# Performance work log

Measured on AMD Instinct MI355X. Metric: run time of the kernel, lower is better.

## Reference

```python
import jax, jax.numpy as jnp
import numpy as np

N_NODES = 100000
N_TYPES = 7
N_EDGES = 400000
D = 128


def setup_inputs() -> dict:
    key = jax.random.key(0)
    k1, k2, k3, k4 = jax.random.split(key, 4)
    x = jax.random.normal(k1, (N_NODES, D), dtype=jnp.float32)
    edge_indices = jax.random.randint(k2, (N_TYPES, 2, N_EDGES), 0, N_NODES, dtype=jnp.int64)
    # per-type linear weights of the cloned base GNNs (scaled for stability)
    W = jax.random.normal(k3, (N_TYPES, D, D), dtype=jnp.float32) * (1.0 / np.sqrt(D))
    b = jax.random.normal(k4, (N_TYPES, D), dtype=jnp.float32) * 0.02
    return {"x": x, "edge_indices": edge_indices, "W": W, "b": b}


def _type_conv(x, src, dst, Wt, bt, n_nodes):
    # gather -> segment-mean aggregate -> linear, one edge type
    msg = x[src]                                                   # [E, D]
    summed = jax.ops.segment_sum(msg, dst, num_segments=n_nodes)   # [N, D]
    cnt = jax.ops.segment_sum(jnp.ones(src.shape, x.dtype), dst, num_segments=n_nodes)
    mean = summed / jnp.maximum(cnt, 1.0)[:, None]
    return mean @ Wt + bt


def reference(x, edge_indices, W, b):
    n_nodes = x.shape[0]
    n_types = edge_indices.shape[0]
    # loop over the small fixed set of edge types (structurally distinct GNNs)
    acc = jnp.zeros_like(x)
    for t in range(n_types):
        acc = acc + _type_conv(x, edge_indices[t, 0], edge_indices[t, 1], W[t], b[t], n_nodes)
    return acc / n_types
```

## Files before the change

### kernel.cpp

```cpp
#include <hip/hip_runtime.h>

#define N_NODES 100000
#define N_TYPES 7
#define N_EDGES 400000
#define DIM 128
#define NTOT (N_TYPES * N_NODES)
#define ETOT (N_TYPES * N_EDGES)

#define RBITS 10
#define RNODE 1024
#define NBUCK 98
#define BSTRIDE 128
#define CAP 6144
#define CHUNK 2048
#define NCHUNKS ((N_EDGES + CHUNK - 1) / CHUNK)

typedef short v8s __attribute__((ext_vector_type(8)));
typedef float v4f __attribute__((ext_vector_type(4)));

__device__ __forceinline__ unsigned short f2bf(float f) {
    unsigned int x = __float_as_uint(f);
    return (unsigned short)((x + 0x7FFFu + ((x >> 16) & 1u)) >> 16);
}

__global__ __launch_bounds__(256) void cast_x_kernel(
    const float* __restrict__ x, unsigned short* __restrict__ xb)
{
    int i = blockIdx.x * 256 + threadIdx.x;
    if (i >= N_NODES * DIM / 4) return;
    float4 v = reinterpret_cast<const float4*>(x)[i];
    ushort4 o;
    o.x = f2bf(v.x); o.y = f2bf(v.y); o.z = f2bf(v.z); o.w = f2bf(v.w);
    reinterpret_cast<ushort4*>(xb)[i] = o;
}

__global__ __launch_bounds__(256) void cast_wt_bsum_kernel(
    const float* __restrict__ W, const float* __restrict__ b,
    unsigned short* __restrict__ WT, float* __restrict__ bsum)
{
    if (blockIdx.x == 448) {
        int j = threadIdx.x;
        if (j < DIM) {
            float s = 0.f;
            for (int t = 0; t < N_TYPES; ++t) s += b[t * DIM + j];
            bsum[j] = s;
        }
        return;
    }
    int i = blockIdx.x * 256 + threadIdx.x;
    if (i >= N_TYPES * DIM * DIM) return;
    int t = i >> 14, r = i & 16383, j = r >> 7, k = r & 127;
    WT[i] = f2bf(W[(t << 14) + (k << 7) + j]);
}

__global__ __launch_bounds__(256) void binpass_kernel(
    const int* __restrict__ ei, int* __restrict__ gcur,
    unsigned int* __restrict__ bucketbuf)
{
    __shared__ unsigned int packedLds[CHUNK];
    __shared__ unsigned char bLds[CHUNK];
    __shared__ unsigned int sortedLds[CHUNK];
    __shared__ int cnt[BSTRIDE];
    __shared__ int lofs[BSTRIDE];
    __shared__ int gbase[BSTRIDE];

    const int blk = blockIdx.x;
    const int t = blk / NCHUNKS;
    const int c = blk - t * NCHUNKS;
    const int* srcp = ei + (size_t)t * 2 * N_EDGES;
    const int* dstp = srcp + N_EDGES;
    const int e0 = c * CHUNK;
    const int e1 = min(e0 + CHUNK, N_EDGES);
    const int tid = threadIdx.x;

    if (tid < BSTRIDE) cnt[tid] = 0;
    __syncthreads();

#pragma unroll
    for (int k = 0; k < CHUNK / 256; ++k) {
        int j = tid + k * 256;
        int e = e0 + j;
        unsigned char b = 0xFF;
        unsigned int pk = 0;
        if (e < e1) {
            int s = srcp[e];
            int d = dstp[e];
            b = (unsigned char)(d >> RBITS);
            pk = ((unsigned int)(d & (RNODE - 1)) << 17) | (unsigned int)s;
            atomicAdd(&cnt[b], 1);
        }
        packedLds[j] = pk;
        bLds[j] = b;
    }
    __syncthreads();

    if (tid < BSTRIDE) lofs[tid] = cnt[tid];
    __syncthreads();
    for (int off = 1; off < BSTRIDE; off <<= 1) {
        int tv = 0;
        if (tid >= off && tid < BSTRIDE) tv = lofs[tid - off];
        __syncthreads();
        if (tid < BSTRIDE) lofs[tid] += tv;
        __syncthreads();
    }
    if (tid < BSTRIDE) lofs[tid] -= cnt[tid];
    __syncthreads();

    if (tid < BSTRIDE) {
        int n = cnt[tid];
        int base = -1;
        if (n > 0 && tid < NBUCK) {
            int rel = atomicAdd(&gcur[t * BSTRIDE + tid], n);
            base = (t * BSTRIDE + tid) * CAP + rel;
        }
        gbase[tid] = base;
        cnt[tid] = lofs[tid];
    }
    __syncthreads();

#pragma unroll
    for (int k = 0; k < CHUNK / 256; ++k) {
        int j = tid + k * 256;
        unsigned char b = bLds[j];
        if (b != 0xFF) {
            int p = atomicAdd(&cnt[b], 1);
            sortedLds[p] = packedLds[j];
        }
    }
    __syncthreads();

    const int wave = tid >> 6, lane = tid & 63;
    for (int b = wave * 32; b < wave * 32 + 32; ++b) {
        if (b >= NBUCK) break;
        int base = gbase[b];
        if (base < 0) continue;
        int o = lofs[b];
        int n = cnt[b] - o;
        for (int i = lane; i < n; i += 64)
            bucketbuf[(size_t)base + i] = sortedLds[o + i];
    }
}

__global__ __launch_bounds__(256) void bucket_hist_scan_kernel(
    const unsigned int* __restrict__ bucketbuf, const int* __restrict__ gcur,
    int* __restrict__ offs, int* __restrict__ bscan)
{
    __shared__ int cnt[RNODE];
    __shared__ int s[256];
    const int blk = blockIdx.x;
    const int t = blk / NBUCK;
    const int b = blk - t * NBUCK;
    const int n = min(gcur[t * BSTRIDE + b], CAP);
    const int g0 = b << RBITS;
    const int validR = min(RNODE, N_NODES - g0);
    const int tid = threadIdx.x;
    for (int j = tid; j < RNODE; j += 256) cnt[j] = 0;
    __syncthreads();
    const unsigned int* bb = bucketbuf + (size_t)(t * BSTRIDE + b) * CAP;
    for (int i = tid; i < n; i += 256)
        atomicAdd(&cnt[bb[i] >> 17], 1);
    __syncthreads();
    int base4 = tid * 4;
    int v[4], tot = 0;
#pragma unroll
    for (int k = 0; k < 4; ++k) { v[k] = cnt[base4 + k]; tot += v[k]; }
    s[tid] = tot;
    __syncthreads();
    for (int off = 1; off < 256; off <<= 1) {
        int t2 = (tid >= off) ? s[tid - off] : 0;
        __syncthreads();
        s[tid] += t2;
        __syncthreads();
    }
    int run = s[tid] - tot;
    int* og = offs + (size_t)t * N_NODES + g0;
#pragma unroll
    for (int k = 0; k < 4; ++k) {
        if (base4 + k < validR) og[base4 + k] = run;
        run += v[k];
    }
    if (tid == 255) bscan[t * NBUCK + b] = s[255];
}

__global__ __launch_bounds__(1024) void scan2_kernel(int* __restrict__ bsum, int nb)
{
    __shared__ int s[1024];
    int tid = threadIdx.x;
    int v = (tid < nb) ? bsum[tid] : 0;
    s[tid] = v;
    __syncthreads();
    for (int off = 1; off < 1024; off <<= 1) {
        int t2 = (tid >= off) ? s[tid - off] : 0;
        __syncthreads();
        s[tid] += t2;
        __syncthreads();
    }
    if (tid < nb) bsum[tid] = s[tid] - v;
}

__global__ __launch_bounds__(256) void scan3_kernel(
    int* __restrict__ offs, const int* __restrict__ bscan)
{
    int i = blockIdx.x * 256 + threadIdx.x;
    if (i < NTOT) {
        int t = i / N_NODES;
        int r = i - t * N_NODES;
        offs[i] += bscan[t * NBUCK + (r >> RBITS)];
    }
    if (i == 0) offs[NTOT] = ETOT;
}

__global__ __launch_bounds__(256) void place_kernel(
    const unsigned int* __restrict__ bucketbuf, const int* __restrict__ gcur,
    const int* __restrict__ offs, int* __restrict__ srcperm)
{
    __shared__ int cur[RNODE];
    __shared__ int sorted[CAP];
    const int blk = blockIdx.x;
    const int t = blk / NBUCK;
    const int b = blk - t * NBUCK;
    const int n = min(gcur[t * BSTRIDE + b], CAP);
    const int g0 = b << RBITS;
    const int validR = min(RNODE, N_NODES - g0);
    const int tid = threadIdx.x;
    const int* offt = offs + (size_t)t * N_NODES + g0;
    const int base0 = offt[0];
    for (int j = tid; j < validR; j += 256) cur[j] = offt[j] - base0;
    __syncthreads();
    const unsigned int* bb = bucketbuf + (size_t)(t * BSTRIDE + b) * CAP;
    for (int i = tid; i < n; i += 256) {
        unsigned int pk = bb[i];
        int p = atomicAdd(&cur[pk >> 17], 1);
        sorted[p] = (int)(pk & 0x1FFFFu);
    }
    __syncthreads();
    int* outp = srcperm + base0;
    for (int i = tid; i < n; i += 256) outp[i] = sorted[i];
}

__global__ __launch_bounds__(256) void aggregate_kernel(
    const unsigned short* __restrict__ xb,
    const int* __restrict__ offs,
    const int* __restrict__ srcperm,
    unsigned short* __restrict__ meanout,
    int grp0, int ngrp)
{
    int gi = blockIdx.x * 16 + (threadIdx.x >> 4);
    if (gi >= ngrp) return;
    int grp = grp0 + gi;
    int l = threadIdx.x & 15;

    int beg = offs[grp];
    int end = offs[grp + 1];
    int m = end - beg;

    int mm = m;
    mm = max(mm, __shfl_xor(mm, 16));
    mm = max(mm, __shfl_xor(mm, 32));

    float a[8];
#pragma unroll
    for (int j = 0; j < 8; ++j) a[j] = 0.f;

    const int eSafe = min(beg, ETOT - 1);
#pragma unroll 4
    for (int i = 0; i < mm; ++i) {
        bool valid = i < m;
        int e = valid ? (beg + i) : eSafe;
        int s = srcperm[e];
        uint4 v = *reinterpret_cast<const uint4*>(
            reinterpret_cast<const char*>(xb) + ((size_t)s << 8) + (l << 4));
        float w = valid ? 1.f : 0.f;
        a[0] += w * __uint_as_float(v.x << 16);
        a[1] += w * __uint_as_float(v.x & 0xFFFF0000u);
        a[2] += w * __uint_as_float(v.y << 16);
        a[3] += w * __uint_as_float(v.y & 0xFFFF0000u);
        a[4] += w * __uint_as_float(v.z << 16);
        a[5] += w * __uint_as_float(v.z & 0xFFFF0000u);
        a[6] += w * __uint_as_float(v.w << 16);
        a[7] += w * __uint_as_float(v.w & 0xFFFF0000u);
    }

    float inv = 1.0f / fmaxf((float)m, 1.0f);
    unsigned int p0, p1, p2, p3;
    asm("v_cvt_pk_bf16_f32 %0, %1, %2" : "=v"(p0) : "v"(a[0] * inv), "v"(a[1] * inv));
    asm("v_cvt_pk_bf16_f32 %0, %1, %2" : "=v"(p1) : "v"(a[2] * inv), "v"(a[3] * inv));
    asm("v_cvt_pk_bf16_f32 %0, %1, %2" : "=v"(p2) : "v"(a[4] * inv), "v"(a[5] * inv));
    asm("v_cvt_pk_bf16_f32 %0, %1, %2" : "=v"(p3) : "v"(a[6] * inv), "v"(a[7] * inv));
    uint4 o = make_uint4(p0, p1, p2, p3);
    *reinterpret_cast<uint4*>(
        reinterpret_cast<char*>(meanout) + ((size_t)gi << 8) + (l << 4)) = o;
}

__global__ __launch_bounds__(256) void matmul_kernel(
    const unsigned short* __restrict__ meanall, size_t meanStride,
    int t0, int nt,
    const unsigned short* __restrict__ WT,
    const float* __restrict__ bsum,
    float* __restrict__ out, int accum)
{
    __shared__ unsigned short sB[DIM * DIM];

    const int tid = threadIdx.x;
    const int wave = tid >> 6;
    const int lane = tid & 63;
    const int rlo = lane & 15;
    const int khi = lane >> 4;
    const int row0 = blockIdx.x * 64 + wave * 16;

    v4f acc[8];
#pragma unroll
    for (int n = 0; n < 8; ++n) acc[n] = (v4f){0.f, 0.f, 0.f, 0.f};

    for (int tt = 0; tt < nt; ++tt) {
        int t = t0 + tt;
        __syncthreads();
        const uint4* gw = reinterpret_cast<const uint4*>(WT + ((size_t)t << 14));
#pragma unroll
        for (int i = 0; i < 8; ++i) {
            int c = tid + (i << 8);
            uint4 v = gw[c];
            int L = c << 4;
            int row = L >> 8;
            int sb = (row << 8) | ((L & 255) ^ ((row & 7) << 4));
            *reinterpret_cast<uint4*>(reinterpret_cast<char*>(sB) + sb) = v;
        }
        __syncthreads();

        int rowA = row0 + rlo;
        if (rowA >= N_NODES) rowA = N_NODES - 1;
        const unsigned short* arow = meanall + (size_t)tt * meanStride + ((size_t)rowA << 7);

#pragma unroll
        for (int k0 = 0; k0 < DIM; k0 += 32) {
            v8s a = *reinterpret_cast<const v8s*>(arow + k0 + (khi << 3));
#pragma unroll
            for (int n = 0; n < 8; ++n) {
                int jrow = (n << 4) | rlo;
                int kb = (k0 + (khi << 3)) << 1;
                int sb = (jrow << 8) | (kb ^ ((jrow & 7) << 4));
                v8s bf = *reinterpret_cast<const v8s*>(reinterpret_cast<char*>(sB) + sb);
                acc[n] = __builtin_amdgcn_mfma_f32_16x16x32_bf16(a, bf, acc[n], 0, 0, 0);
            }
        }
    }

    const float inv7 = 1.0f / 7.0f;
#pragma unroll
    for (int n = 0; n < 8; ++n) {
        int col = (n << 4) | rlo;
        float bs = bsum[col];
#pragma unroll
        for (int r = 0; r < 4; ++r) {
            int row = row0 + (khi << 2) + r;
            if (row < N_NODES) {
                float* p = out + ((size_t)row << 7) + col;
                if (accum) *p += acc[n][r] * inv7;
                else       *p = (acc[n][r] + bs) * inv7;
            }
        }
    }
}

__global__ __launch_bounds__(256) void out_init_kernel(
    const float* __restrict__ bsum, float* __restrict__ out)
{
    int i = blockIdx.x * 256 + threadIdx.x;
    if (i >= N_NODES * DIM / 4) return;
    int c4 = (i & 31) * 4;
    const float inv7 = 1.0f / 7.0f;
    float4 bv = *reinterpret_cast<const float4*>(bsum + c4);
    float4 o = make_float4(bv.x * inv7, bv.y * inv7, bv.z * inv7, bv.w * inv7);
    reinterpret_cast<float4*>(out)[i] = o;
}

extern "C" void kernel_launch(void* const* d_in, const int* in_sizes, int n_in,
                              void* d_out, int out_size, void* d_ws, size_t ws_size,
                              hipStream_t stream) {
    const float* x  = (const float*)d_in[0];
    const int*   ei = (const int*)d_in[1];
    const float* W  = (const float*)d_in[2];
    const float* b  = (const float*)d_in[3];
    float* out = (float*)d_out;

    char* p = (char*)d_ws;
    unsigned short* xb = (unsigned short*)p;          p += (size_t)N_NODES * DIM * 2;
    unsigned short* WT = (unsigned short*)p;          p += (size_t)N_TYPES * DIM * DIM * 2;
    float* bsum = (float*)p;                          p += 512;
    int* srcperm = (int*)p;                           p += (size_t)ETOT * 4;
    int* offs = (int*)p;                              p += (size_t)(NTOT + 1) * 4;
    int* bscan = (int*)p;                             p += 1024 * 4;
    int* gcur = (int*)p;                              p += (size_t)N_TYPES * BSTRIDE * 4;
    p = (char*)(((uintptr_t)p + 15) & ~(uintptr_t)15);
    unsigned int* bucketbuf = (unsigned int*)p;
    unsigned short* meanbuf = (unsigned short*)p;
    size_t mean1_bytes = (size_t)N_NODES * DIM * 2;
    size_t used = (size_t)(p - (char*)d_ws);
    size_t bucket_bytes = (size_t)N_TYPES * BSTRIDE * CAP * 4;
    bool fused = (ws_size >= used + 7 * mean1_bytes) &&
                 (7 * mean1_bytes >= bucket_bytes);

    cast_x_kernel<<<(N_NODES * DIM / 4 + 255) / 256, 256, 0, stream>>>(x, xb);
    cast_wt_bsum_kernel<<<449, 256, 0, stream>>>(W, b, WT, bsum);

    hipMemsetAsync(gcur, 0, (size_t)N_TYPES * BSTRIDE * 4, stream);
    binpass_kernel<<<N_TYPES * NCHUNKS, 256, 0, stream>>>(ei, gcur, bucketbuf);
    bucket_hist_scan_kernel<<<N_TYPES * NBUCK, 256, 0, stream>>>(bucketbuf, gcur, offs, bscan);
    scan2_kernel<<<1, 1024, 0, stream>>>(bscan, N_TYPES * NBUCK);
    scan3_kernel<<<(NTOT + 255) / 256, 256, 0, stream>>>(offs, bscan);
    place_kernel<<<N_TYPES * NBUCK, 256, 0, stream>>>(bucketbuf, gcur, offs, srcperm);

    const int matmul_blocks = (N_NODES + 63) / 64;

    if (fused) {
        size_t meanStride = (size_t)N_NODES * DIM;
        aggregate_kernel<<<(NTOT + 15) / 16, 256, 0, stream>>>(
            xb, offs, srcperm, meanbuf, 0, NTOT);
        matmul_kernel<<<matmul_blocks, 256, 0, stream>>>(
            meanbuf, meanStride, 0, N_TYPES, WT, bsum, out, 0);
    } else {
        out_init_kernel<<<(N_NODES * DIM / 4 + 255) / 256, 256, 0, stream>>>(bsum, out);
        for (int t = 0; t < N_TYPES; ++t) {
            aggregate_kernel<<<(N_NODES + 15) / 16, 256, 0, stream>>>(
                xb, offs, srcperm, meanbuf, t * N_NODES, N_NODES);
            matmul_kernel<<<matmul_blocks, 256, 0, stream>>>(
                meanbuf, 0, t, 1, WT, bsum, out, 1);
        }
    }
}
```

Measured before the change: 243.2 us.

## Fuse CSR histogram, scan and placement; double rows per matmul block

The per-bucket histogram, global scan, offset fixup and placement kernels are replaced by two kernels. One small kernel scans the bucket counts to get each bucket's base. A single fused kernel then loads each bucket into LDS once, builds its histogram, writes the final offsets and scatters the sorted source indices. This removes two launches, the full pass over the offsets array and a second global read of the bucket buffer. Separately, each matmul block now handles 128 rows with two accumulator sets that share each W tile read from LDS, trading more registers and fewer blocks for less W reuse traffic.

```diff
diff --git a/kernel.cpp b/kernel.cpp
--- a/kernel.cpp
+++ b/kernel.cpp
@@ -10,6 +10,7 @@
 #define RBITS 10
 #define RNODE 1024
 #define NBUCK 98
+#define NTB (N_TYPES * NBUCK)
 #define BSTRIDE 128
 #define CAP 6144
 #define CHUNK 2048
@@ -141,25 +142,56 @@
     }
 }
 
-__global__ __launch_bounds__(256) void bucket_hist_scan_kernel(
+__global__ __launch_bounds__(1024) void bucket_base_kernel(
+    const int* __restrict__ gcur, int* __restrict__ sbase, int* __restrict__ offs)
+{
+    __shared__ int s[1024];
+    int tid = threadIdx.x;
+    int v = 0;
+    if (tid < NTB) {
+        int t = tid / NBUCK, b = tid - t * NBUCK;
+        v = min(gcur[t * BSTRIDE + b], CAP);
+    }
+    s[tid] = v;
+    __syncthreads();
+    for (int off = 1; off < 1024; off <<= 1) {
+        int t2 = (tid >= off) ? s[tid - off] : 0;
+        __syncthreads();
+        s[tid] += t2;
+        __syncthreads();
+    }
+    if (tid < NTB) sbase[tid] = s[tid] - v;
+    if (tid == 0) offs[NTOT] = ETOT;
+}
+
+__global__ __launch_bounds__(256) void hist_place_kernel(
     const unsigned int* __restrict__ bucketbuf, const int* __restrict__ gcur,
-    int* __restrict__ offs, int* __restrict__ bscan)
-{
+    const int* __restrict__ sbase,
+    int* __restrict__ offs, int* __restrict__ srcperm)
+{
+    __shared__ unsigned int sorted[CAP];
+    __shared__ unsigned int sorted2[CAP];
     __shared__ int cnt[RNODE];
     __shared__ int s[256];
+
     const int blk = blockIdx.x;
     const int t = blk / NBUCK;
     const int b = blk - t * NBUCK;
     const int n = min(gcur[t * BSTRIDE + b], CAP);
+    const int ebase = sbase[blk];
     const int g0 = b << RBITS;
     const int validR = min(RNODE, N_NODES - g0);
     const int tid = threadIdx.x;
+
+    const unsigned int* bb = bucketbuf + (size_t)(t * BSTRIDE + b) * CAP;
+    for (int i = tid; i < n; i += 256) sorted[i] = bb[i];
     for (int j = tid; j < RNODE; j += 256) cnt[j] = 0;
     __syncthreads();
-    const unsigned int* bb = bucketbuf + (size_t)(t * BSTRIDE + b) * CAP;
+
     for (int i = tid; i < n; i += 256)
-        atomicAdd(&cnt[bb[i] >> 17], 1);
-    __syncthreads();
+        atomicAdd(&cnt[sorted[i] >> 17], 1);
+    __syncthreads();
+
     int base4 = tid * 4;
     int v[4], tot = 0;
 #pragma unroll
@@ -176,66 +208,21 @@
     int* og = offs + (size_t)t * N_NODES + g0;
 #pragma unroll
     for (int k = 0; k < 4; ++k) {
-        if (base4 + k < validR) og[base4 + k] = run;
+        if (base4 + k < validR) og[base4 + k] = ebase + run;
+        cnt[base4 + k] = run;
         run += v[k];
     }
-    if (tid == 255) bscan[t * NBUCK + b] = s[255];
-}
-
-__global__ __launch_bounds__(1024) void scan2_kernel(int* __restrict__ bsum, int nb)
-{
-    __shared__ int s[1024];
-    int tid = threadIdx.x;
-    int v = (tid < nb) ? bsum[tid] : 0;
-    s[tid] = v;
-    __syncthreads();
-    for (int off = 1; off < 1024; off <<= 1) {
-        int t2 = (tid >= off) ? s[tid - off] : 0;
-        __syncthreads();
-        s[tid] += t2;
-        __syncthreads();
-    }
-    if (tid < nb) bsum[tid] = s[tid] - v;
-}
-
-__global__ __launch_bounds__(256) void scan3_kernel(
-    int* __restrict__ offs, const int* __restrict__ bscan)
-{
-    int i = blockIdx.x * 256 + threadIdx.x;
-    if (i < NTOT) {
-        int t = i / N_NODES;
-        int r = i - t * N_NODES;
-        offs[i] += bscan[t * NBUCK + (r >> RBITS)];
-    }
-    if (i == 0) offs[NTOT] = ETOT;
-}
-
-__global__ __launch_bounds__(256) void place_kernel(
-    const unsigned int* __restrict__ bucketbuf, const int* __restrict__ gcur,
-    const int* __restrict__ offs, int* __restrict__ srcperm)
-{
-    __shared__ int cur[RNODE];
-    __shared__ int sorted[CAP];
-    const int blk = blockIdx.x;
-    const int t = blk / NBUCK;
-    const int b = blk - t * NBUCK;
-    const int n = min(gcur[t * BSTRIDE + b], CAP);
-    const int g0 = b << RBITS;
-    const int validR = min(RNODE, N_NODES - g0);
-    const int tid = threadIdx.x;
-    const int* offt = offs + (size_t)t * N_NODES + g0;
-    const int base0 = offt[0];
-    for (int j = tid; j < validR; j += 256) cur[j] = offt[j] - base0;
-    __syncthreads();
-    const unsigned int* bb = bucketbuf + (size_t)(t * BSTRIDE + b) * CAP;
+    __syncthreads();
+
     for (int i = tid; i < n; i += 256) {
-        unsigned int pk = bb[i];
-        int p = atomicAdd(&cur[pk >> 17], 1);
-        sorted[p] = (int)(pk & 0x1FFFFu);
-    }
-    __syncthreads();
-    int* outp = srcperm + base0;
-    for (int i = tid; i < n; i += 256) outp[i] = sorted[i];
+        unsigned int pk = sorted[i];
+        int p = atomicAdd(&cnt[pk >> 17], 1);
+        sorted2[p] = pk & 0x1FFFFu;
+    }
+    __syncthreads();
+
+    int* outp = srcperm + ebase;
+    for (int i = tid; i < n; i += 256) outp[i] = (int)sorted2[i];
 }
 
 __global__ __launch_bounds__(256) void aggregate_kernel(
@@ -306,11 +293,16 @@
     const int lane = tid & 63;
     const int rlo = lane & 15;
     const int khi = lane >> 4;
-    const int row0 = blockIdx.x * 64 + wave * 16;
-
-    v4f acc[8];
-#pragma unroll
-    for (int n = 0; n < 8; ++n) acc[n] = (v4f){0.f, 0.f, 0.f, 0.f};
+    const int row0 = blockIdx.x * 128 + wave * 16;
+
+    v4f acc[2][8];
+#pragma unroll
+    for (int u = 0; u < 2; ++u)
+#pragma unroll
+        for (int n = 0; n < 8; ++n) acc[u][n] = (v4f){0.f, 0.f, 0.f, 0.f};
+
+    int rowA0 = row0 + rlo;       if (rowA0 >= N_NODES) rowA0 = N_NODES - 1;
+    int rowA1 = row0 + 64 + rlo;  if (rowA1 >= N_NODES) rowA1 = N_NODES - 1;
 
     for (int tt = 0; tt < nt; ++tt) {
         int t = t0 + tt;
@@ -327,36 +319,40 @@
         }
         __syncthreads();
 
-        int rowA = row0 + rlo;
-        if (rowA >= N_NODES) rowA = N_NODES - 1;
-        const unsigned short* arow = meanall + (size_t)tt * meanStride + ((size_t)rowA << 7);
+        const unsigned short* ar0 = meanall + (size_t)tt * meanStride + ((size_t)rowA0 << 7);
+        const unsigned short* ar1 = meanall + (size_t)tt * meanStride + ((size_t)rowA1 << 7);
 
 #pragma unroll
         for (int k0 = 0; k0 < DIM; k0 += 32) {
-            v8s a = *reinterpret_cast<const v8s*>(arow + k0 + (khi << 3));
+            v8s a0 = *reinterpret_cast<const v8s*>(ar0 + k0 + (khi << 3));
+            v8s a1 = *reinterpret_cast<const v8s*>(ar1 + k0 + (khi << 3));
 #pragma unroll
             for (int n = 0; n < 8; ++n) {
                 int jrow = (n << 4) | rlo;
                 int kb = (k0 + (khi << 3)) << 1;
                 int sb = (jrow << 8) | (kb ^ ((jrow & 7) << 4));
                 v8s bf = *reinterpret_cast<const v8s*>(reinterpret_cast<char*>(sB) + sb);
-                acc[n] = __builtin_amdgcn_mfma_f32_16x16x32_bf16(a, bf, acc[n], 0, 0, 0);
+                acc[0][n] = __builtin_amdgcn_mfma_f32_16x16x32_bf16(a0, bf, acc[0][n], 0, 0, 0);
+                acc[1][n] = __builtin_amdgcn_mfma_f32_16x16x32_bf16(a1, bf, acc[1][n], 0, 0, 0);
             }
         }
     }
 
     const float inv7 = 1.0f / 7.0f;
 #pragma unroll
-    for (int n = 0; n < 8; ++n) {
-        int col = (n << 4) | rlo;
-        float bs = bsum[col];
-#pragma unroll
-        for (int r = 0; r < 4; ++r) {
-            int row = row0 + (khi << 2) + r;
-            if (row < N_NODES) {
-                float* p = out + ((size_t)row << 7) + col;
-                if (accum) *p += acc[n][r] * inv7;
-                else       *p = (acc[n][r] + bs) * inv7;
+    for (int u = 0; u < 2; ++u) {
+#pragma unroll
+        for (int n = 0; n < 8; ++n) {
+            int col = (n << 4) | rlo;
+            float bs = bsum[col];
+#pragma unroll
+            for (int r = 0; r < 4; ++r) {
+                int row = row0 + u * 64 + (khi << 2) + r;
+                if (row < N_NODES) {
+                    float* p = out + ((size_t)row << 7) + col;
+                    if (accum) *p += acc[u][n][r] * inv7;
+                    else       *p = (acc[u][n][r] + bs) * inv7;
+                }
             }
         }
     }
@@ -389,7 +385,7 @@
     float* bsum = (float*)p;                          p += 512;
     int* srcperm = (int*)p;                           p += (size_t)ETOT * 4;
     int* offs = (int*)p;                              p += (size_t)(NTOT + 1) * 4;
-    int* bscan = (int*)p;                             p += 1024 * 4;
+    int* sbase = (int*)p;                             p += 1024 * 4;
     int* gcur = (int*)p;                              p += (size_t)N_TYPES * BSTRIDE * 4;
     p = (char*)(((uintptr_t)p + 15) & ~(uintptr_t)15);
     unsigned int* bucketbuf = (unsigned int*)p;
@@ -405,12 +401,10 @@
 
     hipMemsetAsync(gcur, 0, (size_t)N_TYPES * BSTRIDE * 4, stream);
     binpass_kernel<<<N_TYPES * NCHUNKS, 256, 0, stream>>>(ei, gcur, bucketbuf);
-    bucket_hist_scan_kernel<<<N_TYPES * NBUCK, 256, 0, stream>>>(bucketbuf, gcur, offs, bscan);
-    scan2_kernel<<<1, 1024, 0, stream>>>(bscan, N_TYPES * NBUCK);
-    scan3_kernel<<<(NTOT + 255) / 256, 256, 0, stream>>>(offs, bscan);
-    place_kernel<<<N_TYPES * NBUCK, 256, 0, stream>>>(bucketbuf, gcur, offs, srcperm);
-
-    const int matmul_blocks = (N_NODES + 63) / 64;
+    bucket_base_kernel<<<1, 1024, 0, stream>>>(gcur, sbase, offs);
+    hist_place_kernel<<<NTB, 256, 0, stream>>>(bucketbuf, gcur, sbase, offs, srcperm);
+
+    const int matmul_blocks = (N_NODES + 127) / 128;
 
     if (fused) {
         size_t meanStride = (size_t)N_NODES * DIM;
```

Result: no change. 246.0 us (+1.2%).
